# Performance work log

Hardware: AMD Instinct MI355X
Metric: run time of the kernel (lower is better)

## Reference

```python
import jax, jax.numpy as jnp
import numpy as np

D_MODEL = 256
N_HEADS = 8
N_LEVELS = 4
N_POINTS = 4
DH = D_MODEL // N_HEADS
SHAPES = [(100, 150), (50, 75), (25, 38), (13, 19)]  # per-level (H, W)
BATCH = 2


def setup_inputs() -> dict:
    key = jax.random.key(0)
    ks = jax.random.split(key, 8)
    Lq = sum(h * w for h, w in SHAPES)  # 19947
    d = D_MODEL
    off_dim = N_HEADS * N_LEVELS * N_POINTS * 2
    aw_dim = N_HEADS * N_LEVELS * N_POINTS
    s = 1.0 / np.sqrt(d).astype(np.float32)
    lsi = np.concatenate([[0], np.cumsum([h * w for h, w in SHAPES])[:-1]])
    return {
        "query": jax.random.normal(ks[0], (BATCH, Lq, d), jnp.float32),
        "reference_points": jax.random.uniform(ks[1], (BATCH, Lq, N_LEVELS, 2), jnp.float32),
        "input_flatten": jax.random.normal(ks[2], (BATCH, Lq, d), jnp.float32),
        "input_spatial_shapes": jnp.array(SHAPES, dtype=jnp.int32),
        "input_level_start_index": jnp.array(lsi, dtype=jnp.int32),
        "W_samp": 0.01 * jax.random.normal(ks[3], (off_dim, d), jnp.float32),
        "b_samp": 0.1 * jax.random.normal(ks[4], (off_dim,), jnp.float32),
        "W_attn": s * jax.random.normal(ks[5], (aw_dim, d), jnp.float32),
        "b_attn": jnp.zeros((aw_dim,), jnp.float32),
        "W_val": s * jax.random.normal(ks[6], (d, d), jnp.float32),
        "b_val": jnp.zeros((d,), jnp.float32),
        "W_out": s * jax.random.normal(ks[7], (d, d), jnp.float32),
        "b_out": jnp.zeros((d,), jnp.float32),
    }


def _bilinear(v, grid, Hl, Wl):
    # v: [N, H, Hl*Wl, Dh] flattened level feature map per head
    # grid: [N, H, Q, P, 2] in [-1, 1]; align_corners=False, zero padding
    N, H, Q, P, _ = grid.shape
    Dh = v.shape[-1]
    x = (grid[..., 0] + 1.0) * 0.5 * Wl - 0.5
    y = (grid[..., 1] + 1.0) * 0.5 * Hl - 0.5
    x0 = jnp.floor(x)
    y0 = jnp.floor(y)
    lx = x - x0
    ly = y - y0
    x0i = x0.astype(jnp.int32)
    y0i = y0.astype(jnp.int32)

    def corner(xi, yi, w):
        valid = (xi >= 0) & (xi < Wl) & (yi >= 0) & (yi < Hl)
        idx = jnp.clip(yi, 0, Hl - 1) * Wl + jnp.clip(xi, 0, Wl - 1)
        g = jnp.take_along_axis(v, idx.reshape(N, H, Q * P, 1), axis=2)
        return g.reshape(N, H, Q, P, Dh) * (w * valid)[..., None]

    return (corner(x0i, y0i, (1 - lx) * (1 - ly))
            + corner(x0i + 1, y0i, lx * (1 - ly))
            + corner(x0i, y0i + 1, (1 - lx) * ly)
            + corner(x0i + 1, y0i + 1, lx * ly))


def _forward(query, ref, x, shapes, W_samp, b_samp, W_attn, b_attn, W_val, b_val, W_out, b_out):
    N, Lq, d = query.shape
    H, L, P, Dh = N_HEADS, N_LEVELS, N_POINTS, DH
    # value projection -> [N, H, S, Dh]
    value = (x @ W_val.T + b_val).reshape(N, -1, H, Dh).transpose(0, 2, 1, 3)
    off = (query @ W_samp.T + b_samp).reshape(N, Lq, H, L, P, 2)
    attw = jax.nn.softmax((query @ W_attn.T + b_attn).reshape(N, Lq, H, L * P), axis=-1)
    attw = attw.reshape(N, Lq, H, L, P).transpose(0, 2, 1, 3, 4)  # [N,H,Lq,L,P]
    # offset normalizer is (W, H) per level
    norm = jnp.array([[w, h] for h, w in shapes], dtype=query.dtype)  # [L, 2]
    loc = ref[:, :, None, :, None, :] + off / norm[None, None, None, :, None, :]
    grids = (2.0 * loc - 1.0).transpose(0, 2, 1, 3, 4, 5)  # [N,H,Lq,L,P,2]

    acc = jnp.zeros((N, Lq, H, Dh), query.dtype)
    start = 0
    for lvl, (Hl, Wl) in enumerate(shapes):
        v = value[:, :, start:start + Hl * Wl]  # [N,H,Hl*Wl,Dh]
        start += Hl * Wl
        samp = _bilinear(v, grids[:, :, :, lvl], Hl, Wl)  # [N,H,Lq,P,Dh]
        acc = acc + jnp.einsum('nhqpd,nhqp->nqhd', samp, attw[:, :, :, lvl])
    out = acc.reshape(N, Lq, H * Dh)
    return out @ W_out.T + b_out


def reference(query, reference_points, input_flatten, input_spatial_shapes,
              input_level_start_index, W_samp, b_samp, W_attn, b_attn,
              W_val, b_val, W_out, b_out):
    shapes = [(int(h), int(w)) for h, w in np.asarray(input_spatial_shapes)]
    return _forward(query, reference_points, input_flatten, shapes,
                    W_samp, b_samp, W_attn, b_attn, W_val, b_val, W_out, b_out)
```

## Files before the change

### kernel.cpp

```cpp
#include <hip/hip_runtime.h>
#include <hip/hip_bf16.h>

#define NB 2
#define LQ 19947
#define LV 19947
#define DM 256
#define NH 8
#define NL 4
#define NP 4
#define MROWS (NB*LQ)
#define MPAD  39936
#define QPB 2

__device__ __constant__ int c_lvlH[4] = {100, 50, 25, 13};
__device__ __constant__ int c_lvlW[4] = {150, 75, 38, 19};
__device__ __constant__ int c_lvlS[4] = {0, 15000, 18750, 19700};

typedef __attribute__((ext_vector_type(8))) short short8;
typedef __attribute__((ext_vector_type(4))) float f32x4;

__device__ __forceinline__ unsigned short f2bf(float f) {
  unsigned u = __float_as_uint(f);
  u += 0x7FFFu + ((u >> 16) & 1u);
  return (unsigned short)(u >> 16);
}
__device__ __forceinline__ float bfl(unsigned u) { return __uint_as_float(u << 16); }
__device__ __forceinline__ float bfh(unsigned u) { return __uint_as_float(u & 0xFFFF0000u); }

#define CB_X 9984
__global__ __launch_bounds__(256) void conv_all(
    const float* __restrict__ xin, const float* __restrict__ query,
    const float* __restrict__ Wv, const float* __restrict__ Wsamp,
    const float* __restrict__ Wattn, const float* __restrict__ Wout,
    const float* __restrict__ bsamp, const float* __restrict__ battn,
    unsigned short* __restrict__ xb, unsigned short* __restrict__ qb,
    unsigned short* __restrict__ wvb, unsigned short* __restrict__ wqb,
    unsigned short* __restrict__ wob, float* __restrict__ bsa)
{
  const int b = blockIdx.x, t = threadIdx.x;
  if (b == 2 * CB_X + 224) {
    bsa[t] = bsamp[t];
    if (t < 128) bsa[256 + t] = battn[t];
    return;
  }
  const float* src; unsigned short* dst; int base, ns;
  if (b < CB_X)            { src = xin;   dst = xb;          base = b * 1024;                ns = MROWS * 256; }
  else if (b < 2*CB_X)     { src = query; dst = qb;          base = (b - CB_X) * 1024;       ns = MROWS * 256; }
  else if (b < 2*CB_X+64)  { src = Wv;    dst = wvb;         base = (b - 2*CB_X) * 1024;     ns = 65536; }
  else if (b < 2*CB_X+128) { src = Wsamp; dst = wqb;         base = (b - 2*CB_X-64) * 1024;  ns = 65536; }
  else if (b < 2*CB_X+160) { src = Wattn; dst = wqb + 65536; base = (b - 2*CB_X-128) * 1024; ns = 32768; }
  else                     { src = Wout;  dst = wob;         base = (b - 2*CB_X-160) * 1024; ns = 65536; }
  const int i = base + t * 4;
  ushort4 o;
  if (i + 4 <= ns) {
    const float4 v = *(const float4*)(src + i);
    o.x = f2bf(v.x); o.y = f2bf(v.y); o.z = f2bf(v.z); o.w = f2bf(v.w);
  } else {
    float vs[4];
    #pragma unroll
    for (int j = 0; j < 4; ++j) vs[j] = (i + j < ns) ? src[i + j] : 0.f;
    o.x = f2bf(vs[0]); o.y = f2bf(vs[1]); o.z = f2bf(vs[2]); o.w = f2bf(vs[3]);
  }
  *(ushort4*)(dst + i) = o;
}

__global__ __launch_bounds__(256) void gemm_front(
    const unsigned short* __restrict__ xb, const unsigned short* __restrict__ qb,
    const unsigned short* __restrict__ wvb, const unsigned short* __restrict__ wqb,
    const float* __restrict__ b_val, const float* __restrict__ bsa,
    unsigned short* __restrict__ value, unsigned short* __restrict__ oc)
{
  const unsigned short* Ab; const unsigned short* Wb; const float* bias;
  unsigned short* Cp; int Nn, cb;
  if (blockIdx.y < 2) { Ab = xb; Wb = wvb; bias = b_val; Cp = value; Nn = 256; cb = blockIdx.y; }
  else                { Ab = qb; Wb = wqb; bias = bsa;   Cp = oc;    Nn = 384; cb = blockIdx.y - 2; }

  __shared__ alignas(16) short As[128 * 32];
  __shared__ alignas(16) short Bs[128 * 32];

  const int t = threadIdx.x;
  const int w = t >> 6, l = t & 63;
  const int wr = w >> 1, wc = w & 1;
  const size_t rowBase = (size_t)blockIdx.x * 128;
  const int colBase = cb * 128;

  const f32x4 z = {0.f, 0.f, 0.f, 0.f};
  f32x4 acc[4][4];
  #pragma unroll
  for (int i = 0; i < 4; ++i)
    #pragma unroll
    for (int j = 0; j < 4; ++j) acc[i][j] = z;

  const int srow = l >> 2;
  const int scol = (l & 3) * 8;

  for (int ks = 0; ks < 8; ++ks) {
    const int k0 = ks * 32;
    #pragma unroll
    for (int i = 0; i < 2; ++i) {
      const int ii = w * 2 + i;
      const unsigned short* gA = Ab + (rowBase + ii * 16 + srow) * 256 + k0 + scol;
      __builtin_amdgcn_global_load_lds(
          (const __attribute__((address_space(1))) void*)gA,
          (__attribute__((address_space(3))) void*)&As[ii * 512], 16, 0, 0);
      const unsigned short* gB = Wb + ((size_t)(colBase + ii * 16 + srow)) * 256 + k0 + scol;
      __builtin_amdgcn_global_load_lds(
          (const __attribute__((address_space(1))) void*)gB,
          (__attribute__((address_space(3))) void*)&Bs[ii * 512], 16, 0, 0);
    }
    __syncthreads();
    short8 af[4], bf[4];
    #pragma unroll
    for (int i = 0; i < 4; ++i) {
      af[i] = *(const short8*)&As[(wr * 64 + i * 16 + (l & 15)) * 32 + (l >> 4) * 8];
      bf[i] = *(const short8*)&Bs[(wc * 64 + i * 16 + (l & 15)) * 32 + (l >> 4) * 8];
    }
    #pragma unroll
    for (int i = 0; i < 4; ++i)
      #pragma unroll
      for (int j = 0; j < 4; ++j)
        acc[i][j] = __builtin_amdgcn_mfma_f32_16x16x32_bf16(bf[j], af[i], acc[i][j], 0, 0, 0);
    __syncthreads();
  }

  const int row0 = (int)rowBase + wr * 64 + (l & 15);
  const int col0 = colBase + wc * 64 + (l >> 4) * 4;
  #pragma unroll
  for (int j = 0; j < 4; ++j) {
    const float4 bj = *(const float4*)(bias + col0 + j * 16);
    #pragma unroll
    for (int i = 0; i < 4; ++i) {
      const int row = row0 + i * 16;
      uint2 st;
      st.x = (unsigned)f2bf(acc[i][j][0] + bj.x) | ((unsigned)f2bf(acc[i][j][1] + bj.y) << 16);
      st.y = (unsigned)f2bf(acc[i][j][2] + bj.z) | ((unsigned)f2bf(acc[i][j][3] + bj.w) << 16);
      *(uint2*)(Cp + (size_t)row * Nn + col0 + j * 16) = st;
    }
  }
}

__global__ __launch_bounds__(256) void gemm_out(
    const unsigned short* __restrict__ Ab, const unsigned short* __restrict__ Wb,
    const float* __restrict__ bias, float* __restrict__ Cp)
{
  __shared__ alignas(16) short As[128 * 32];
  __shared__ alignas(16) short Bs[128 * 32];

  const int t = threadIdx.x;
  const int w = t >> 6, l = t & 63;
  const int wr = w >> 1, wc = w & 1;
  const size_t rowBase = (size_t)blockIdx.x * 128;
  const int colBase = blockIdx.y * 128;

  const f32x4 z = {0.f, 0.f, 0.f, 0.f};
  f32x4 acc[4][4];
  #pragma unroll
  for (int i = 0; i < 4; ++i)
    #pragma unroll
    for (int j = 0; j < 4; ++j) acc[i][j] = z;

  const int srow = l >> 2;
  const int scol = (l & 3) * 8;

  for (int ks = 0; ks < 8; ++ks) {
    const int k0 = ks * 32;
    #pragma unroll
    for (int i = 0; i < 2; ++i) {
      const int ii = w * 2 + i;
      const unsigned short* gA = Ab + (rowBase + ii * 16 + srow) * 256 + k0 + scol;
      __builtin_amdgcn_global_load_lds(
          (const __attribute__((address_space(1))) void*)gA,
          (__attribute__((address_space(3))) void*)&As[ii * 512], 16, 0, 0);
      const unsigned short* gB = Wb + ((size_t)(colBase + ii * 16 + srow)) * 256 + k0 + scol;
      __builtin_amdgcn_global_load_lds(
          (const __attribute__((address_space(1))) void*)gB,
          (__attribute__((address_space(3))) void*)&Bs[ii * 512], 16, 0, 0);
    }
    __syncthreads();
    short8 af[4], bf[4];
    #pragma unroll
    for (int i = 0; i < 4; ++i) {
      af[i] = *(const short8*)&As[(wr * 64 + i * 16 + (l & 15)) * 32 + (l >> 4) * 8];
      bf[i] = *(const short8*)&Bs[(wc * 64 + i * 16 + (l & 15)) * 32 + (l >> 4) * 8];
    }
    #pragma unroll
    for (int i = 0; i < 4; ++i)
      #pragma unroll
      for (int j = 0; j < 4; ++j)
        acc[i][j] = __builtin_amdgcn_mfma_f32_16x16x32_bf16(bf[j], af[i], acc[i][j], 0, 0, 0);
    __syncthreads();
  }

  const int row0 = (int)rowBase + wr * 64 + (l & 15);
  const int col0 = colBase + wc * 64 + (l >> 4) * 4;
  #pragma unroll
  for (int j = 0; j < 4; ++j) {
    const float4 bj = *(const float4*)(bias + col0 + j * 16);
    #pragma unroll
    for (int i = 0; i < 4; ++i) {
      const int row = row0 + i * 16;
      if (row < MROWS) {
        *(float4*)(Cp + (size_t)row * 256 + col0 + j * 16) =
            make_float4(acc[i][j][0] + bj.x, acc[i][j][1] + bj.y,
                        acc[i][j][2] + bj.z, acc[i][j][3] + bj.w);
      }
    }
  }
}

__global__ __launch_bounds__(128) void msda_sample(
    const unsigned short* __restrict__ value,
    const float* __restrict__ refp,
    const unsigned short* __restrict__ oc,
    unsigned short* __restrict__ accb)
{
  __shared__ float s_aw[QPB][128];
  __shared__ float s_ref[QPB][8];
  __shared__ alignas(16) unsigned s_poff[QPB][NH][17][4];
  __shared__ alignas(16) float    s_pw[QPB][NH][17][4];

  const int t = threadIdx.x;
  const int bq0 = blockIdx.x * QPB;

  {
    const int q = t >> 6, i = t & 63;
    const int bq = bq0 + q;
    const unsigned pw = *(const unsigned*)(oc + (size_t)bq * 384 + 256 + i * 2);
    s_aw[q][i * 2 + 0] = bfl(pw);
    s_aw[q][i * 2 + 1] = bfh(pw);
    if (t < QPB * 8) {
      const int q2 = t >> 3, j = t & 7;
      s_ref[q2][j] = refp[(size_t)(bq0 + q2) * 8 + j];
    }
  }
  __syncthreads();

  if (t < QPB * NH) {
    const int q = t >> 3, h = t & 7;
    float* aw = &s_aw[q][h * 16];
    float m = aw[0];
    #pragma unroll
    for (int i = 1; i < 16; ++i) m = fmaxf(m, aw[i]);
    float e[16]; float s = 0.f;
    #pragma unroll
    for (int i = 0; i < 16; ++i) { e[i] = __expf(aw[i] - m); s += e[i]; }
    const float inv = 1.f / s;
    #pragma unroll
    for (int i = 0; i < 16; ++i) aw[i] = e[i] * inv;
  }
  __syncthreads();

  #pragma unroll
  for (int it = t; it < QPB * 128; it += 128) {
    const int q = it >> 7, rem = it & 127;
    const int h = rem >> 4, idx = rem & 15;
    const int l = idx >> 2;
    const int bq = bq0 + q;
    const unsigned po = *(const unsigned*)(oc + (size_t)bq * 384 + rem * 2);
    const int Hl = c_lvlH[l], Wl = c_lvlW[l], st = c_lvlS[l];
    const float x = s_ref[q][l * 2 + 0] * (float)Wl - 0.5f + bfl(po);
    const float y = s_ref[q][l * 2 + 1] * (float)Hl - 0.5f + bfh(po);
    const float aw = s_aw[q][rem];
    const float x0f = floorf(x), y0f = floorf(y);
    const float lx = x - x0f, ly = y - y0f;
    const int x0 = (int)x0f, y0 = (int)y0f;
    const float vx0 = (x0 >= 0 && x0 < Wl) ? 1.f : 0.f;
    const float vx1 = (x0 >= -1 && x0 < Wl - 1) ? 1.f : 0.f;
    const float vy0 = (y0 >= 0 && y0 < Hl) ? 1.f : 0.f;
    const float vy1 = (y0 >= -1 && y0 < Hl - 1) ? 1.f : 0.f;
    const int xc0 = min(max(x0, 0), Wl - 1);
    const int xc1 = min(max(x0 + 1, 0), Wl - 1);
    const int yc0 = min(max(y0, 0), Hl - 1);
    const int yc1 = min(max(y0 + 1, 0), Hl - 1);
    const int r0 = st + yc0 * Wl, r1 = st + yc1 * Wl;
    s_poff[q][h][idx][0] = (unsigned)(r0 + xc0) * 512u;
    s_poff[q][h][idx][1] = (unsigned)(r0 + xc1) * 512u;
    s_poff[q][h][idx][2] = (unsigned)(r1 + xc0) * 512u;
    s_poff[q][h][idx][3] = (unsigned)(r1 + xc1) * 512u;
    s_pw[q][h][idx][0] = (1.f - lx) * (1.f - ly) * aw * (vx0 * vy0);
    s_pw[q][h][idx][1] = lx * (1.f - ly) * aw * (vx1 * vy0);
    s_pw[q][h][idx][2] = (1.f - lx) * ly * aw * (vx0 * vy1);
    s_pw[q][h][idx][3] = lx * ly * aw * (vx1 * vy1);
  }
  __syncthreads();

  const int w = t >> 6;
  const int lane = t & 63;
  const int bq = bq0 + w;
  const int n = bq / LQ;
  const char* vbase = (const char*)value + (size_t)n * LV * 512;
  const int h = lane >> 3;
  const int laneoff = h * 64 + (lane & 7) * 8;

  float a0 = 0.f, a1 = 0.f, a2 = 0.f, a3 = 0.f;
  #pragma unroll
  for (int idx = 0; idx < 16; ++idx) {
    const uint4  of = *(const uint4*)&s_poff[w][h][idx][0];
    const float4 wt = *(const float4*)&s_pw[w][h][idx][0];
    const uint2 p00 = *(const uint2*)(vbase + (of.x + laneoff));
    const uint2 p10 = *(const uint2*)(vbase + (of.y + laneoff));
    const uint2 p01 = *(const uint2*)(vbase + (of.z + laneoff));
    const uint2 p11 = *(const uint2*)(vbase + (of.w + laneoff));
    a0 += wt.x * bfl(p00.x) + wt.y * bfl(p10.x) + wt.z * bfl(p01.x) + wt.w * bfl(p11.x);
    a1 += wt.x * bfh(p00.x) + wt.y * bfh(p10.x) + wt.z * bfh(p01.x) + wt.w * bfh(p11.x);
    a2 += wt.x * bfl(p00.y) + wt.y * bfl(p10.y) + wt.z * bfl(p01.y) + wt.w * bfl(p11.y);
    a3 += wt.x * bfh(p00.y) + wt.y * bfh(p10.y) + wt.z * bfh(p01.y) + wt.w * bfh(p11.y);
  }
  ushort4 o;
  o.x = f2bf(a0); o.y = f2bf(a1); o.z = f2bf(a2); o.w = f2bf(a3);
  *(ushort4*)(accb + (size_t)bq * 256 + lane * 4) = o;
}

extern "C" void kernel_launch(void* const* d_in, const int* in_sizes, int n_in,
                              void* d_out, int out_size, void* d_ws, size_t ws_size,
                              hipStream_t stream) {
  const float* query  = (const float*)d_in[0];
  const float* refp   = (const float*)d_in[1];
  const float* xin    = (const float*)d_in[2];
  const float* W_samp = (const float*)d_in[5];
  const float* b_samp = (const float*)d_in[6];
  const float* W_attn = (const float*)d_in[7];
  const float* b_attn = (const float*)d_in[8];
  const float* W_val  = (const float*)d_in[9];
  const float* b_val  = (const float*)d_in[10];
  const float* W_out  = (const float*)d_in[11];
  const float* b_out  = (const float*)d_in[12];
  float* out = (float*)d_out;
  (void)in_sizes; (void)n_in; (void)out_size; (void)ws_size;

  char* ws = (char*)d_ws;
  unsigned short* value = (unsigned short*)(ws);
  unsigned short* qb    = (unsigned short*)(ws + 20447232);
  unsigned short* xb    = (unsigned short*)(ws + 40894464);
  unsigned short* accb  = xb;
  unsigned short* oc    = (unsigned short*)(ws + 61341696);
  unsigned short* wvb   = (unsigned short*)(ws + 92012544);
  unsigned short* wqb   = (unsigned short*)(ws + 92143616);
  unsigned short* wob   = (unsigned short*)(ws + 92340224);
  float*          bsa   = (float*)(ws + 92471296);

  hipLaunchKernelGGL(conv_all, dim3(2 * CB_X + 225), dim3(256), 0, stream,
                     xin, query, W_val, W_samp, W_attn, W_out, b_samp, b_attn,
                     xb, qb, wvb, wqb, wob, bsa);
  hipLaunchKernelGGL(gemm_front, dim3(312, 5), dim3(256), 0, stream,
                     xb, qb, wvb, wqb, b_val, bsa, value, oc);
  hipLaunchKernelGGL(msda_sample, dim3(MROWS / QPB), dim3(128), 0, stream,
                     value, refp, oc, accb);
  hipLaunchKernelGGL(gemm_out, dim3(312, 2), dim3(256), 0, stream,
                     accb, wob, b_out, out);
}
```

Baseline: 284.5 us.

## Widen sampling gathers to 16B, split corners across lanes, software-pipeline loads

Reorganizes the sampling loop so each lane loads 16 bytes (8 bf16 channels) for two of the four bilinear corners, with lane pairs covering the other two corners and combining results via a cross-lane shuffle. Offsets and weights are packed together in shared memory so each lane reads one uint4, and global gathers are prefetched three iterations ahead in a rotating register pipeline. Accumulation uses packed float2 math. The aim is fewer, wider memory transactions and better latency hiding, at the cost of more registers and an extra shuffle reduction.

```diff
diff --git a/kernel.cpp b/kernel.cpp
--- a/kernel.cpp
+++ b/kernel.cpp
@@ -18,6 +18,7 @@
 
 typedef __attribute__((ext_vector_type(8))) short short8;
 typedef __attribute__((ext_vector_type(4))) float f32x4;
+typedef __attribute__((ext_vector_type(2))) float f32x2;
 
 __device__ __forceinline__ unsigned short f2bf(float f) {
   unsigned u = __float_as_uint(f);
@@ -26,6 +27,9 @@
 }
 __device__ __forceinline__ float bfl(unsigned u) { return __uint_as_float(u << 16); }
 __device__ __forceinline__ float bfh(unsigned u) { return __uint_as_float(u & 0xFFFF0000u); }
+__device__ __forceinline__ f32x2 up2(unsigned u) {
+  f32x2 r; r.x = __uint_as_float(u << 16); r.y = __uint_as_float(u & 0xFFFF0000u); return r;
+}
 
 #define CB_X 9984
 __global__ __launch_bounds__(256) void conv_all(
@@ -216,8 +220,7 @@
 {
   __shared__ float s_aw[QPB][128];
   __shared__ float s_ref[QPB][8];
-  __shared__ alignas(16) unsigned s_poff[QPB][NH][17][4];
-  __shared__ alignas(16) float    s_pw[QPB][NH][17][4];
+  __shared__ alignas(16) unsigned s_pk[QPB][NH][17][8];
 
   const int t = threadIdx.x;
   const int bq0 = blockIdx.x * QPB;
@@ -273,42 +276,76 @@
     const int yc0 = min(max(y0, 0), Hl - 1);
     const int yc1 = min(max(y0 + 1, 0), Hl - 1);
     const int r0 = st + yc0 * Wl, r1 = st + yc1 * Wl;
-    s_poff[q][h][idx][0] = (unsigned)(r0 + xc0) * 512u;
-    s_poff[q][h][idx][1] = (unsigned)(r0 + xc1) * 512u;
-    s_poff[q][h][idx][2] = (unsigned)(r1 + xc0) * 512u;
-    s_poff[q][h][idx][3] = (unsigned)(r1 + xc1) * 512u;
-    s_pw[q][h][idx][0] = (1.f - lx) * (1.f - ly) * aw * (vx0 * vy0);
-    s_pw[q][h][idx][1] = lx * (1.f - ly) * aw * (vx1 * vy0);
-    s_pw[q][h][idx][2] = (1.f - lx) * ly * aw * (vx0 * vy1);
-    s_pw[q][h][idx][3] = lx * ly * aw * (vx1 * vy1);
+    uint4 g0, g1;
+    g0.x = (unsigned)(r0 + xc0) * 512u;
+    g0.y = (unsigned)(r0 + xc1) * 512u;
+    g0.z = __float_as_uint((1.f - lx) * (1.f - ly) * aw * (vx0 * vy0));
+    g0.w = __float_as_uint(lx * (1.f - ly) * aw * (vx1 * vy0));
+    g1.x = (unsigned)(r1 + xc0) * 512u;
+    g1.y = (unsigned)(r1 + xc1) * 512u;
+    g1.z = __float_as_uint((1.f - lx) * ly * aw * (vx0 * vy1));
+    g1.w = __float_as_uint(lx * ly * aw * (vx1 * vy1));
+    *(uint4*)&s_pk[q][h][idx][0] = g0;
+    *(uint4*)&s_pk[q][h][idx][4] = g1;
   }
   __syncthreads();
 
-  const int w = t >> 6;
+  const int wv = t >> 6;
   const int lane = t & 63;
-  const int bq = bq0 + w;
+  const int bq = bq0 + wv;
   const int n = bq / LQ;
   const char* vbase = (const char*)value + (size_t)n * LV * 512;
   const int h = lane >> 3;
-  const int laneoff = h * 64 + (lane & 7) * 8;
-
-  float a0 = 0.f, a1 = 0.f, a2 = 0.f, a3 = 0.f;
+  const int c2 = (lane >> 2) & 1;
+  const unsigned laneoff = (unsigned)(h * 64 + (lane & 3) * 16);
+
+  f32x2 acc0 = {0.f, 0.f}, acc1 = {0.f, 0.f}, acc2 = {0.f, 0.f}, acc3 = {0.f, 0.f};
+
+#define PKRD(i) (*(const uint4*)&s_pk[wv][h][(i)][c2 * 4])
+#define GLD(o)  (*(const uint4*)(vbase + (o) + laneoff))
+
+  uint4 pk0 = PKRD(0), pk1 = PKRD(1), pk2 = PKRD(2), pk3 = PKRD(3);
+  uint4 va0 = GLD(pk0.x), vb0 = GLD(pk0.y);
+  uint4 va1 = GLD(pk1.x), vb1 = GLD(pk1.y);
+  uint4 va2 = GLD(pk2.x), vb2 = GLD(pk2.y);
+
   #pragma unroll
   for (int idx = 0; idx < 16; ++idx) {
-    const uint4  of = *(const uint4*)&s_poff[w][h][idx][0];
-    const float4 wt = *(const float4*)&s_pw[w][h][idx][0];
-    const uint2 p00 = *(const uint2*)(vbase + (of.x + laneoff));
-    const uint2 p10 = *(const uint2*)(vbase + (of.y + laneoff));
-    const uint2 p01 = *(const uint2*)(vbase + (of.z + laneoff));
-    const uint2 p11 = *(const uint2*)(vbase + (of.w + laneoff));
-    a0 += wt.x * bfl(p00.x) + wt.y * bfl(p10.x) + wt.z * bfl(p01.x) + wt.w * bfl(p11.x);
-    a1 += wt.x * bfh(p00.x) + wt.y * bfh(p10.x) + wt.z * bfh(p01.x) + wt.w * bfh(p11.x);
-    a2 += wt.x * bfl(p00.y) + wt.y * bfl(p10.y) + wt.z * bfl(p01.y) + wt.w * bfl(p11.y);
-    a3 += wt.x * bfh(p00.y) + wt.y * bfh(p10.y) + wt.z * bfh(p01.y) + wt.w * bfh(p11.y);
-  }
-  ushort4 o;
-  o.x = f2bf(a0); o.y = f2bf(a1); o.z = f2bf(a2); o.w = f2bf(a3);
-  *(ushort4*)(accb + (size_t)bq * 256 + lane * 4) = o;
+    uint4 va3, vb3, pk4;
+    if (idx < 13) { va3 = GLD(pk3.x); vb3 = GLD(pk3.y); }
+    if (idx < 12) { pk4 = PKRD(idx + 4); }
+    const float was = __uint_as_float(pk0.z);
+    const float wbs = __uint_as_float(pk0.w);
+    f32x2 wa; wa.x = was; wa.y = was;
+    f32x2 wb; wb.x = wbs; wb.y = wbs;
+    acc0 = acc0 + wa * up2(va0.x);
+    acc1 = acc1 + wa * up2(va0.y);
+    acc2 = acc2 + wa * up2(va0.z);
+    acc3 = acc3 + wa * up2(va0.w);
+    acc0 = acc0 + wb * up2(vb0.x);
+    acc1 = acc1 + wb * up2(vb0.y);
+    acc2 = acc2 + wb * up2(vb0.z);
+    acc3 = acc3 + wb * up2(vb0.w);
+    pk0 = pk1; pk1 = pk2; pk2 = pk3; pk3 = pk4;
+    va0 = va1; va1 = va2; va2 = va3;
+    vb0 = vb1; vb1 = vb2; vb2 = vb3;
+  }
+#undef PKRD
+#undef GLD
+
+  acc0.x += __shfl_xor(acc0.x, 4); acc0.y += __shfl_xor(acc0.y, 4);
+  acc1.x += __shfl_xor(acc1.x, 4); acc1.y += __shfl_xor(acc1.y, 4);
+  acc2.x += __shfl_xor(acc2.x, 4); acc2.y += __shfl_xor(acc2.y, 4);
+  acc3.x += __shfl_xor(acc3.x, 4); acc3.y += __shfl_xor(acc3.y, 4);
+
+  if (c2 == 0) {
+    uint4 st;
+    st.x = (unsigned)f2bf(acc0.x) | ((unsigned)f2bf(acc0.y) << 16);
+    st.y = (unsigned)f2bf(acc1.x) | ((unsigned)f2bf(acc1.y) << 16);
+    st.z = (unsigned)f2bf(acc2.x) | ((unsigned)f2bf(acc2.y) << 16);
+    st.w = (unsigned)f2bf(acc3.x) | ((unsigned)f2bf(acc3.y) << 16);
+    *(uint4*)((char*)accb + (size_t)bq * 512 + laneoff) = st;
+  }
 }
 
 extern "C" void kernel_launch(void* const* d_in, const int* in_sizes, int n_in,
```

After: 247.0 us. 1.15x faster.
